# Kernel optimization log

Measured on AMD Instinct MI355X. Metric: run time of the kernel, lower is better.

The kernel has to match this reference:

```python
import jax, jax.numpy as jnp
import numpy as np

N_NODES = 20000
N_EDGES = 320000


def gcn_conv(x, W, b, src, dst, n_nodes):
    """PyG GCNConv: add self-loops, symmetric D^-1/2 (A+I) D^-1/2 normalization,
    linear transform then normalized scatter-add aggregation, plus bias."""
    x = x @ W  # [N, out]
    loop = jnp.arange(n_nodes, dtype=src.dtype)
    s = jnp.concatenate([src, loop])  # [E+N]
    d = jnp.concatenate([dst, loop])
    # degree of destination nodes (edge weight = 1), including self-loops
    deg = jax.ops.segment_sum(jnp.ones_like(d, dtype=x.dtype), d, num_segments=n_nodes)
    dinv = jnp.where(deg > 0, jax.lax.rsqrt(deg), 0.0)
    norm = dinv[s] * dinv[d]  # [E+N]
    msg = x[s] * norm[:, None]  # gather + scale, [E+N, out]
    out = jax.ops.segment_sum(msg, d, num_segments=n_nodes)  # scatter-add
    return out + b


def setup_inputs() -> dict:
    key = jax.random.key(0)
    ks = jax.random.split(key, 8)
    x = jax.random.normal(ks[0], (N_NODES, 10), dtype=jnp.float32)
    edge_index = jax.random.randint(ks[1], (2, N_EDGES), 0, N_NODES, dtype=jnp.int32)
    # Glorot-ish init for weights, zero bias (as in PyG defaults)
    def glorot(k, shape):
        lim = float(np.sqrt(6.0 / (shape[0] + shape[1])))
        return jax.random.uniform(k, shape, jnp.float32, -lim, lim)
    return {
        "x": x,
        "edge_index": edge_index,
        "W1": glorot(ks[2], (10, 256)),
        "b1": jnp.zeros((256,), jnp.float32),
        "W2": glorot(ks[3], (256, 128)),
        "b2": jnp.zeros((128,), jnp.float32),
        "W3": glorot(ks[4], (128, 1)),
        "b3": jnp.zeros((1,), jnp.float32),
    }


def reference(x, edge_index, W1, b1, W2, b2, W3, b3):
    src, dst = edge_index[0], edge_index[1]
    n = x.shape[0]
    h = jax.nn.relu(gcn_conv(x, W1, b1, src, dst, n))
    h = jax.nn.relu(gcn_conv(h, W2, b2, src, dst, n))
    out = gcn_conv(h, W3, b3, src, dst, n)
    return out.squeeze(-1)  # [N]
```

## Files before the change

kernel.cpp:

```cpp
#include <hip/hip_runtime.h>
#include <hip/hip_fp16.h>


constexpr int NN  = 20000;
constexpr int NE  = 320000;
constexpr int F0  = 10;
constexpr int F1  = 256;
constexpr int F2  = 128;
constexpr int MB  = 16;
constexpr int CAP = 64;
constexpr int EMAX = 48;


__global__ void k_fill(const int* __restrict__ src, const int* __restrict__ dst,
                       int* cursor, int* __restrict__ col) {
  int e = blockIdx.x * 256 + threadIdx.x;
  if (e >= NE) return;
  const int d = dst[e], s = src[e];
  const int pos = atomicAdd(&cursor[d], 1) & (CAP - 1);
  col[d * CAP + pos] = s;
}


__global__ __launch_bounds__(256) void k_gemm12(
    const float* __restrict__ x, const int* __restrict__ cursor,
    const int* __restrict__ col, const float* __restrict__ W1,
    const float* __restrict__ b1, const float* __restrict__ W2,
    __half* __restrict__ t2h) {
  __shared__ float alds[MB * F0];
  __shared__ float h1[MB][F1 + 4];
  __shared__ float w2lds[32 * F2];
  __shared__ int   es[MB][EMAX];
  __shared__ float ew[MB][EMAX];
  const int tid = threadIdx.x;
  const int n0 = blockIdx.x * MB;
  float4 pf0 = *((const float4*)W2 + tid);
  float4 pf1 = *((const float4*)W2 + tid + 256);
  float4 pf2 = *((const float4*)W2 + tid + 512);
  float4 pf3 = *((const float4*)W2 + tid + 768);
  {
    const int m = tid >> 4;
    const int j0 = tid & 15;
    const int n = n0 + m;
    const int deg = min(cursor[n], EMAX);
    const int base = n * CAP;
    for (int j = j0; j < deg; j += 16) {
      const int s = col[base + j];
      es[m][j] = s;
      ew[m][j] = rsqrtf((float)(cursor[s] + 1));
    }
  }
  __syncthreads();
  {
    const int m = tid >> 4;
    const int f = tid & 15;
    if (f < F0) {
      const int n = n0 + m;
      const int deg = min(cursor[n], EMAX);
      const float di = rsqrtf((float)(cursor[n] + 1));
      float acc = x[n * F0 + f] * di;
      int j = 0;
      for (; j + 3 < deg; j += 4) {
        const int s0 = es[m][j],     s1 = es[m][j + 1];
        const int s2 = es[m][j + 2], s3 = es[m][j + 3];
        const float q0 = ew[m][j],     q1 = ew[m][j + 1];
        const float q2 = ew[m][j + 2], q3 = ew[m][j + 3];
        acc += x[s0 * F0 + f] * q0 + x[s1 * F0 + f] * q1 +
               x[s2 * F0 + f] * q2 + x[s3 * F0 + f] * q3;
      }
      for (; j < deg; ++j) acc += x[es[m][j] * F0 + f] * ew[m][j];
      alds[m * F0 + f] = di * acc;
    }
  }
  __syncthreads();
  {
    const int c = tid;
    float w1r[F0];
#pragma unroll
    for (int k = 0; k < F0; ++k) w1r[k] = W1[k * F1 + c];
    const float bb = b1[c];
#pragma unroll
    for (int m = 0; m < MB; ++m) {
      float acc = bb;
#pragma unroll
      for (int k = 0; k < F0; ++k) acc += alds[m * F0 + k] * w1r[k];
      h1[m][c] = fmaxf(acc, 0.f);
    }
  }
  const int cg_ = tid & 31;
  const int m0 = (tid >> 5) * 2;
  float a00 = 0.f, a01 = 0.f, a02 = 0.f, a03 = 0.f;
  float a10 = 0.f, a11 = 0.f, a12 = 0.f, a13 = 0.f;
#define FMA4(av, bv, vw)                                            \
  a00 += (av) * (vw).x; a01 += (av) * (vw).y;                       \
  a02 += (av) * (vw).z; a03 += (av) * (vw).w;                       \
  a10 += (bv) * (vw).x; a11 += (bv) * (vw).y;                       \
  a12 += (bv) * (vw).z; a13 += (bv) * (vw).w;
  for (int kc = 0; kc < F1 / 32; ++kc) {
    __syncthreads();
    {
      float4* ldst = (float4*)w2lds;
      ldst[tid] = pf0;
      ldst[tid + 256] = pf1;
      ldst[tid + 512] = pf2;
      ldst[tid + 768] = pf3;
    }
    __syncthreads();
    if (kc + 1 < F1 / 32) {
      const float4* gnext = (const float4*)(W2 + (kc + 1) * 32 * F2);
      pf0 = gnext[tid];
      pf1 = gnext[tid + 256];
      pf2 = gnext[tid + 512];
      pf3 = gnext[tid + 768];
    }
#pragma unroll
    for (int kk = 0; kk < 32; kk += 4) {
      const int k = kc * 32 + kk;
      const float4 ha = *(const float4*)&h1[m0][k];
      const float4 hb = *(const float4*)&h1[m0 + 1][k];
      const float4 w0 = *(const float4*)&w2lds[(kk + 0) * F2 + cg_ * 4];
      const float4 w1v = *(const float4*)&w2lds[(kk + 1) * F2 + cg_ * 4];
      const float4 w2v = *(const float4*)&w2lds[(kk + 2) * F2 + cg_ * 4];
      const float4 w3v = *(const float4*)&w2lds[(kk + 3) * F2 + cg_ * 4];
      FMA4(ha.x, hb.x, w0);
      FMA4(ha.y, hb.y, w1v);
      FMA4(ha.z, hb.z, w2v);
      FMA4(ha.w, hb.w, w3v);
    }
  }
#undef FMA4
  const float d0 = rsqrtf((float)(cursor[n0 + m0] + 1));
  const float d1 = rsqrtf((float)(cursor[n0 + m0 + 1] + 1));
  union PK { uint2 u; __half2 h[2]; };
  PK p0; p0.h[0] = __floats2half2_rn(a00 * d0, a01 * d0);
         p0.h[1] = __floats2half2_rn(a02 * d0, a03 * d0);
  PK p1; p1.h[0] = __floats2half2_rn(a10 * d1, a11 * d1);
         p1.h[1] = __floats2half2_rn(a12 * d1, a13 * d1);
  *(uint2*)&t2h[(size_t)(n0 + m0) * F2 + cg_ * 4] = p0.u;
  *(uint2*)&t2h[(size_t)(n0 + m0 + 1) * F2 + cg_ * 4] = p1.u;
}


__device__ inline void acc_h4(uint2 u, float& a0, float& a1, float& a2, float& a3) {
  union { uint2 u; __half2 h[2]; } pk;
  pk.u = u;
  const float2 f0 = __half22float2(pk.h[0]);
  const float2 f1 = __half22float2(pk.h[1]);
  a0 += f0.x; a1 += f0.y; a2 += f1.x; a3 += f1.y;
}

__global__ __launch_bounds__(256) void k_agg2(
    const __half* __restrict__ t2h, const int* __restrict__ cursor,
    const int* __restrict__ col, const float* __restrict__ b2,
    const float* __restrict__ W3, float* __restrict__ t3s) {
  const int wave = (blockIdx.x * 256 + threadIdx.x) >> 6;
  const int lane = threadIdx.x & 63;
  const int half = lane >> 5;
  const int li   = lane & 31;
  const int n    = wave * 2 + half;
  if (n >= NN) return;
  const int deg = cursor[n];
  const int base = n * CAP;
  const int fx = li * 4;
  float a0 = 0.f, a1 = 0.f, a2 = 0.f, a3 = 0.f;
  acc_h4(*(const uint2*)&t2h[(size_t)n * F2 + fx], a0, a1, a2, a3);
  int k = 0;
  for (; k + 7 < deg; k += 8) {
    const int s0 = col[base + k],     s1 = col[base + k + 1];
    const int s2 = col[base + k + 2], s3 = col[base + k + 3];
    const int s4 = col[base + k + 4], s5 = col[base + k + 5];
    const int s6 = col[base + k + 6], s7 = col[base + k + 7];
    const uint2 v0 = *(const uint2*)&t2h[(size_t)s0 * F2 + fx];
    const uint2 v1 = *(const uint2*)&t2h[(size_t)s1 * F2 + fx];
    const uint2 v2 = *(const uint2*)&t2h[(size_t)s2 * F2 + fx];
    const uint2 v3 = *(const uint2*)&t2h[(size_t)s3 * F2 + fx];
    const uint2 v4 = *(const uint2*)&t2h[(size_t)s4 * F2 + fx];
    const uint2 v5 = *(const uint2*)&t2h[(size_t)s5 * F2 + fx];
    const uint2 v6 = *(const uint2*)&t2h[(size_t)s6 * F2 + fx];
    const uint2 v7 = *(const uint2*)&t2h[(size_t)s7 * F2 + fx];
    acc_h4(v0, a0, a1, a2, a3); acc_h4(v1, a0, a1, a2, a3);
    acc_h4(v2, a0, a1, a2, a3); acc_h4(v3, a0, a1, a2, a3);
    acc_h4(v4, a0, a1, a2, a3); acc_h4(v5, a0, a1, a2, a3);
    acc_h4(v6, a0, a1, a2, a3); acc_h4(v7, a0, a1, a2, a3);
  }
  for (; k + 3 < deg; k += 4) {
    const int s0 = col[base + k],     s1 = col[base + k + 1];
    const int s2 = col[base + k + 2], s3 = col[base + k + 3];
    const uint2 v0 = *(const uint2*)&t2h[(size_t)s0 * F2 + fx];
    const uint2 v1 = *(const uint2*)&t2h[(size_t)s1 * F2 + fx];
    const uint2 v2 = *(const uint2*)&t2h[(size_t)s2 * F2 + fx];
    const uint2 v3 = *(const uint2*)&t2h[(size_t)s3 * F2 + fx];
    acc_h4(v0, a0, a1, a2, a3); acc_h4(v1, a0, a1, a2, a3);
    acc_h4(v2, a0, a1, a2, a3); acc_h4(v3, a0, a1, a2, a3);
  }
  for (; k < deg; ++k) {
    acc_h4(*(const uint2*)&t2h[(size_t)col[base + k] * F2 + fx], a0, a1, a2, a3);
  }
  const float di = rsqrtf((float)(deg + 1));
  const float4 bb = *(const float4*)&b2[fx];
  const float4 w3 = *(const float4*)&W3[fx];
  const float h0 = fmaxf(di * a0 + bb.x, 0.f);
  const float h1 = fmaxf(di * a1 + bb.y, 0.f);
  const float h2 = fmaxf(di * a2 + bb.z, 0.f);
  const float h3 = fmaxf(di * a3 + bb.w, 0.f);
  float p = (h0 * w3.x + h1 * w3.y) + (h2 * w3.z + h3 * w3.w);
#pragma unroll
  for (int off = 16; off > 0; off >>= 1) p += __shfl_down(p, off);
  if (li == 0) t3s[n] = di * p;
}


__global__ __launch_bounds__(256) void k_agg3(
    const float* __restrict__ t3s, const int* __restrict__ cursor,
    const int* __restrict__ col, const float* __restrict__ b3,
    float* __restrict__ out) {
  const int wave = (blockIdx.x * 256 + threadIdx.x) >> 6;
  const int lane = threadIdx.x & 63;
  const int sub  = lane >> 4;
  const int li   = lane & 15;
  const int n    = wave * 4 + sub;
  if (n >= NN) return;
  const int deg = cursor[n];
  const int base = n * CAP;
  float acc = 0.f;
  for (int j = li; j < deg; j += 16) acc += t3s[col[base + j]];
  acc += __shfl_xor(acc, 8);
  acc += __shfl_xor(acc, 4);
  acc += __shfl_xor(acc, 2);
  acc += __shfl_xor(acc, 1);
  if (li == 0)
    out[n] = rsqrtf((float)(deg + 1)) * (acc + t3s[n]) + b3[0];
}

extern "C" void kernel_launch(void* const* d_in, const int* in_sizes, int n_in,
                              void* d_out, int out_size, void* d_ws, size_t ws_size,
                              hipStream_t stream) {
  const float* x = (const float*)d_in[0];
  const int* ei = (const int*)d_in[1];
  const int* srcv = ei;
  const int* dstv = ei + NE;
  const float* W1 = (const float*)d_in[2];
  const float* b1 = (const float*)d_in[3];
  const float* W2 = (const float*)d_in[4];
  const float* b2 = (const float*)d_in[5];
  const float* W3 = (const float*)d_in[6];
  const float* b3 = (const float*)d_in[7];
  float* out = (float*)d_out;

  char* w = (char*)d_ws;
  auto alloc = [&](size_t bytes) -> void* {
    void* p = (void*)w;
    w += (bytes + 255) & ~(size_t)255;
    return p;
  };
  int*    cursor = (int*)   alloc(NN * 4);
  int*    col    = (int*)   alloc((size_t)NN * CAP * 4);
  __half* t2h    = (__half*)alloc((size_t)NN * F2 * 2);
  float*  t3s    = (float*) alloc(NN * 4);

  (void)hipMemsetAsync(cursor, 0, NN * 4, stream);
  k_fill<<<(NE + 255) / 256, 256, 0, stream>>>(srcv, dstv, cursor, col);
  k_gemm12<<<NN / MB, 256, 0, stream>>>(x, cursor, col, W1, b1, W2, t2h);
  k_agg2<<<NN / 8, 256, 0, stream>>>(t2h, cursor, col, b2, W3, t3s);
  k_agg3<<<(NN + 15) / 16, 256, 0, stream>>>(t3s, cursor, col, b3, out);
}
```

Measured before the change: 137.7 us.

## Use fp16 MFMA for second-layer GEMM with pre-transposed half-precision W2

Replaces the scalar fp32 FMA loop for the h1·W2 product with MFMA 16x16x32 f16 instructions. A new small kernel transposes W2 and casts it to fp16, and h1 is kept in LDS as fp16 with padded strides. The per-node degree normalizer is also cached in LDS. The aim is to cut ALU time in the GEMM stage, at the cost of an extra kernel launch and lower input precision for the GEMM.

```diff
diff --git a/kernel.cpp b/kernel.cpp
--- a/kernel.cpp
+++ b/kernel.cpp
@@ -11,6 +11,13 @@
 constexpr int CAP = 64;
 constexpr int EMAX = 48;
 
+typedef _Float16 f16x8 __attribute__((ext_vector_type(8)));
+typedef float    f32x4 __attribute__((ext_vector_type(4)));
+
+constexpr int H1S = 264;
+constexpr int BKC = 64;
+constexpr int W2S = 72;
+
 
 __global__ void k_fill(const int* __restrict__ src, const int* __restrict__ dst,
                        int* cursor, int* __restrict__ col) {
@@ -22,28 +29,42 @@
 }
 
 
+__global__ __launch_bounds__(256) void k_w2t(const float* __restrict__ W2,
+                                             _Float16* __restrict__ W2t) {
+  const int t = blockIdx.x * 256 + threadIdx.x;
+  const int n = t >> 8;
+  const int k = t & 255;
+  W2t[n * 256 + k] = (_Float16)W2[k * F2 + n];
+}
+
+
 __global__ __launch_bounds__(256) void k_gemm12(
     const float* __restrict__ x, const int* __restrict__ cursor,
     const int* __restrict__ col, const float* __restrict__ W1,
-    const float* __restrict__ b1, const float* __restrict__ W2,
-    __half* __restrict__ t2h) {
+    const float* __restrict__ b1, const _Float16* __restrict__ W2t,
+    _Float16* __restrict__ t2h) {
   __shared__ float alds[MB * F0];
-  __shared__ float h1[MB][F1 + 4];
-  __shared__ float w2lds[32 * F2];
+  __shared__ float din[MB];
+  __shared__ __align__(16) _Float16 h1h[MB * H1S];
+  __shared__ __align__(16) _Float16 w2t[F2 * W2S];
   __shared__ int   es[MB][EMAX];
   __shared__ float ew[MB][EMAX];
   const int tid = threadIdx.x;
   const int n0 = blockIdx.x * MB;
-  float4 pf0 = *((const float4*)W2 + tid);
-  float4 pf1 = *((const float4*)W2 + tid + 256);
-  float4 pf2 = *((const float4*)W2 + tid + 512);
-  float4 pf3 = *((const float4*)W2 + tid + 768);
+  const uint4* W2t4 = (const uint4*)W2t;
+  const int gb = ((tid >> 3) << 5) + (tid & 7);
+  uint4 pf0 = W2t4[gb];
+  uint4 pf1 = W2t4[gb + 1024];
+  uint4 pf2 = W2t4[gb + 2048];
+  uint4 pf3 = W2t4[gb + 3072];
   {
     const int m = tid >> 4;
     const int j0 = tid & 15;
     const int n = n0 + m;
-    const int deg = min(cursor[n], EMAX);
+    const int degraw = cursor[n];
+    const int deg = min(degraw, EMAX);
     const int base = n * CAP;
+    if (j0 == 0) din[m] = rsqrtf((float)(degraw + 1));
     for (int j = j0; j < deg; j += 16) {
       const int s = col[base + j];
       es[m][j] = s;
@@ -57,7 +78,7 @@
     if (f < F0) {
       const int n = n0 + m;
       const int deg = min(cursor[n], EMAX);
-      const float di = rsqrtf((float)(cursor[n] + 1));
+      const float di = din[m];
       float acc = x[n * F0 + f] * di;
       int j = 0;
       for (; j + 3 < deg; j += 4) {
@@ -84,60 +105,49 @@
       float acc = bb;
 #pragma unroll
       for (int k = 0; k < F0; ++k) acc += alds[m * F0 + k] * w1r[k];
-      h1[m][c] = fmaxf(acc, 0.f);
-    }
-  }
-  const int cg_ = tid & 31;
-  const int m0 = (tid >> 5) * 2;
-  float a00 = 0.f, a01 = 0.f, a02 = 0.f, a03 = 0.f;
-  float a10 = 0.f, a11 = 0.f, a12 = 0.f, a13 = 0.f;
-#define FMA4(av, bv, vw)                                            \
-  a00 += (av) * (vw).x; a01 += (av) * (vw).y;                       \
-  a02 += (av) * (vw).z; a03 += (av) * (vw).w;                       \
-  a10 += (bv) * (vw).x; a11 += (bv) * (vw).y;                       \
-  a12 += (bv) * (vw).z; a13 += (bv) * (vw).w;
-  for (int kc = 0; kc < F1 / 32; ++kc) {
+      h1h[m * H1S + c] = (_Float16)fmaxf(acc, 0.f);
+    }
+  }
+  const int lane = tid & 63;
+  const int wv   = tid >> 6;
+  const int lr   = lane & 15;
+  const int lg   = lane >> 4;
+  const int nt0  = wv * 32;
+  f32x4 acc0 = {0.f, 0.f, 0.f, 0.f};
+  f32x4 acc1 = {0.f, 0.f, 0.f, 0.f};
+  uint4* w2t4 = (uint4*)w2t;
+  const int sb = (tid >> 3) * 9 + (tid & 7);
+  for (int kc = 0; kc < F1 / BKC; ++kc) {
     __syncthreads();
-    {
-      float4* ldst = (float4*)w2lds;
-      ldst[tid] = pf0;
-      ldst[tid + 256] = pf1;
-      ldst[tid + 512] = pf2;
-      ldst[tid + 768] = pf3;
-    }
+    w2t4[sb]       = pf0;
+    w2t4[sb + 288] = pf1;
+    w2t4[sb + 576] = pf2;
+    w2t4[sb + 864] = pf3;
     __syncthreads();
-    if (kc + 1 < F1 / 32) {
-      const float4* gnext = (const float4*)(W2 + (kc + 1) * 32 * F2);
-      pf0 = gnext[tid];
-      pf1 = gnext[tid + 256];
-      pf2 = gnext[tid + 512];
-      pf3 = gnext[tid + 768];
-    }
-#pragma unroll
-    for (int kk = 0; kk < 32; kk += 4) {
-      const int k = kc * 32 + kk;
-      const float4 ha = *(const float4*)&h1[m0][k];
-      const float4 hb = *(const float4*)&h1[m0 + 1][k];
-      const float4 w0 = *(const float4*)&w2lds[(kk + 0) * F2 + cg_ * 4];
-      const float4 w1v = *(const float4*)&w2lds[(kk + 1) * F2 + cg_ * 4];
-      const float4 w2v = *(const float4*)&w2lds[(kk + 2) * F2 + cg_ * 4];
-      const float4 w3v = *(const float4*)&w2lds[(kk + 3) * F2 + cg_ * 4];
-      FMA4(ha.x, hb.x, w0);
-      FMA4(ha.y, hb.y, w1v);
-      FMA4(ha.z, hb.z, w2v);
-      FMA4(ha.w, hb.w, w3v);
-    }
-  }
-#undef FMA4
-  const float d0 = rsqrtf((float)(cursor[n0 + m0] + 1));
-  const float d1 = rsqrtf((float)(cursor[n0 + m0 + 1] + 1));
-  union PK { uint2 u; __half2 h[2]; };
-  PK p0; p0.h[0] = __floats2half2_rn(a00 * d0, a01 * d0);
-         p0.h[1] = __floats2half2_rn(a02 * d0, a03 * d0);
-  PK p1; p1.h[0] = __floats2half2_rn(a10 * d1, a11 * d1);
-         p1.h[1] = __floats2half2_rn(a12 * d1, a13 * d1);
-  *(uint2*)&t2h[(size_t)(n0 + m0) * F2 + cg_ * 4] = p0.u;
-  *(uint2*)&t2h[(size_t)(n0 + m0 + 1) * F2 + cg_ * 4] = p1.u;
+    if (kc + 1 < F1 / BKC) {
+      const uint4* gnext = W2t4 + (kc + 1) * 8;
+      pf0 = gnext[gb];
+      pf1 = gnext[gb + 1024];
+      pf2 = gnext[gb + 2048];
+      pf3 = gnext[gb + 3072];
+    }
+#pragma unroll
+    for (int ks = 0; ks < 2; ++ks) {
+      const int kb = kc * BKC + ks * 32;
+      const f16x8 av = *(const f16x8*)&h1h[lr * H1S + kb + lg * 8];
+      const f16x8 b0 = *(const f16x8*)&w2t[(nt0 + lr) * W2S + ks * 32 + lg * 8];
+      const f16x8 b1v = *(const f16x8*)&w2t[(nt0 + 16 + lr) * W2S + ks * 32 + lg * 8];
+      acc0 = __builtin_amdgcn_mfma_f32_16x16x32_f16(av, b0, acc0, 0, 0, 0);
+      acc1 = __builtin_amdgcn_mfma_f32_16x16x32_f16(av, b1v, acc1, 0, 0, 0);
+    }
+  }
+#pragma unroll
+  for (int r = 0; r < 4; ++r) {
+    const int row = lg * 4 + r;
+    const float dn = din[row];
+    t2h[(size_t)(n0 + row) * F2 + nt0 + lr]      = (_Float16)(acc0[r] * dn);
+    t2h[(size_t)(n0 + row) * F2 + nt0 + 16 + lr] = (_Float16)(acc1[r] * dn);
+  }
 }
 
 
@@ -253,14 +263,16 @@
     w += (bytes + 255) & ~(size_t)255;
     return p;
   };
-  int*    cursor = (int*)   alloc(NN * 4);
-  int*    col    = (int*)   alloc((size_t)NN * CAP * 4);
-  __half* t2h    = (__half*)alloc((size_t)NN * F2 * 2);
-  float*  t3s    = (float*) alloc(NN * 4);
+  int*      cursor = (int*)     alloc(NN * 4);
+  int*      col    = (int*)     alloc((size_t)NN * CAP * 4);
+  _Float16* t2h    = (_Float16*)alloc((size_t)NN * F2 * 2);
+  float*    t3s    = (float*)   alloc(NN * 4);
+  _Float16* W2t    = (_Float16*)alloc((size_t)F2 * F1 * 2);
 
   (void)hipMemsetAsync(cursor, 0, NN * 4, stream);
   k_fill<<<(NE + 255) / 256, 256, 0, stream>>>(srcv, dstv, cursor, col);
-  k_gemm12<<<NN / MB, 256, 0, stream>>>(x, cursor, col, W1, b1, W2, t2h);
-  k_agg2<<<NN / 8, 256, 0, stream>>>(t2h, cursor, col, b2, W3, t3s);
+  k_w2t<<<(F1 * F2) / 256, 256, 0, stream>>>(W2, W2t);
+  k_gemm12<<<NN / MB, 256, 0, stream>>>(x, cursor, col, W1, b1, W2t, t2h);
+  k_agg2<<<NN / 8, 256, 0, stream>>>((const __half*)t2h, cursor, col, b2, W3, t3s);
   k_agg3<<<(NN + 15) / 16, 256, 0, stream>>>(t3s, cursor, col, b3, out);
 }
```

New measurement: 124.4 us. 1.11x faster.
